# Performance work log

Measured on AMD Instinct MI355X. Metric: run time of the kernel, lower is better.

## Reference

```python
import jax, jax.numpy as jnp
import numpy as np

C = 256
RED = 8
CK = C // RED  # 32


def setup_inputs() -> dict:
    key = jax.random.key(0)
    ks = jax.random.split(key, 7)
    x = jax.random.normal(ks[0], (4, C, 64, 64), dtype=jnp.float32)
    s = 1.0 / np.sqrt(C)
    key_W = jax.random.uniform(ks[1], (CK, C), minval=-s, maxval=s, dtype=jnp.float32)
    key_b = jax.random.uniform(ks[2], (CK,), minval=-s, maxval=s, dtype=jnp.float32)
    query_W = jax.random.uniform(ks[3], (CK, C), minval=-s, maxval=s, dtype=jnp.float32)
    query_b = jax.random.uniform(ks[4], (CK,), minval=-s, maxval=s, dtype=jnp.float32)
    value_W = jax.random.uniform(ks[5], (C, C), minval=-s, maxval=s, dtype=jnp.float32)
    value_b = jax.random.uniform(ks[6], (C,), minval=-s, maxval=s, dtype=jnp.float32)
    alpha = jnp.zeros((1,), dtype=jnp.float32)
    return {"x": x, "key_W": key_W, "key_b": key_b, "query_W": query_W,
            "query_b": query_b, "value_W": value_W, "value_b": value_b,
            "alpha": alpha}


def reference(x, key_W, key_b, query_W, query_b, value_W, value_b, alpha):
    B, Cc, H, W = x.shape
    N = H * W
    xf = x.reshape(B, Cc, N)  # [B, C, N]
    # 1x1 convs == per-pixel linear projections
    k = jnp.einsum('kc,bcn->bkn', key_W, xf) + key_b[None, :, None]     # [B, CK, N]
    q = jnp.einsum('kc,bcn->bkn', query_W, xf) + query_b[None, :, None]  # [B, CK, N]
    v = jnp.einsum('oc,bcn->bon', value_W, xf) + value_b[None, :, None]  # [B, C, N]
    # energy[b, i, j] = key_i . query_j
    energy = jnp.einsum('bki,bkj->bij', k, q)  # [B, N, N]
    attn = jax.nn.softmax(energy, axis=-1)
    # out[b, c, i] = sum_j v[b, c, j] * attn[b, i, j]
    out = jnp.einsum('bcj,bij->bci', v, attn)  # [B, C, N]
    out = out.reshape(B, Cc, H, W)
    return alpha * out + x
```

## Files before the change

### kernel.cpp

```cpp
#include <hip/hip_runtime.h>

#define C_DIM 256
#define CK_DIM 32
#define NPIX 4096
#define BATCH 4

typedef __attribute__((ext_vector_type(8))) short bf16x8;
typedef __attribute__((ext_vector_type(4))) float f32x4;
typedef __attribute__((ext_vector_type(16))) float f32x16;
typedef __attribute__((ext_vector_type(4))) unsigned short us4;

__device__ __forceinline__ unsigned short f2bf(float f) {
    union { float f; unsigned int u; } c; c.f = f;
    unsigned int r = c.u + 0x7FFFu + ((c.u >> 16) & 1u);
    return (unsigned short)(r >> 16);
}

__global__ __launch_bounds__(256) void wprep_kernel(
    const float* __restrict__ kW, const float* __restrict__ qW,
    const float* __restrict__ vW, unsigned short* __restrict__ wbf)
{
    int i4 = (blockIdx.x * 256 + threadIdx.x) * 4;
    int o = i4 >> 8, c = i4 & 255;
    const float* src = (o < 32) ? kW + o * 256 + c
                     : (o < 64) ? qW + (o - 32) * 256 + c
                                : vW + (o - 64) * 256 + c;
    float4 f = *(const float4*)src;
    us4 p; p.x = f2bf(f.x); p.y = f2bf(f.y); p.z = f2bf(f.z); p.w = f2bf(f.w);
    *(us4*)&wbf[i4] = p;
}

#define XP 264
__global__ __launch_bounds__(256) void proj_kernel(
    const float* __restrict__ x,
    const unsigned short* __restrict__ wbf,
    const float* __restrict__ key_b, const float* __restrict__ query_b,
    const float* __restrict__ value_b,
    unsigned short* __restrict__ kT,
    unsigned short* __restrict__ qT,
    unsigned short* __restrict__ vt)
{
    const int b  = blockIdx.y;
    const int n0 = blockIdx.x * 64;
    const int t  = threadIdx.x;
    const int w    = t >> 6;
    const int lane = t & 63;
    const int mrow = lane & 15;
    const int quad = lane >> 4;

    __shared__ __align__(16) unsigned short smem[28928];
    #define XT(n, c)      smem[(n) * XP + (c)]
    #define VS(w_, c, nn) smem[(w_) * 6144 + (c) * 24 + (nn)]
    #define KQS(n, o)     smem[24576 + (n) * 68 + (o)]

    const float* xb = x + (size_t)b * C_DIM * NPIX + n0;
    const int cb = (t >> 4) * 4;
    const int n4 = (t & 15) * 4;
    #pragma unroll
    for (int it = 0; it < 4; ++it) {
        int c0 = it * 64 + cb;
        float4 r0 = *(const float4*)(xb + (size_t)(c0 + 0) * NPIX + n4);
        float4 r1 = *(const float4*)(xb + (size_t)(c0 + 1) * NPIX + n4);
        float4 r2 = *(const float4*)(xb + (size_t)(c0 + 2) * NPIX + n4);
        float4 r3 = *(const float4*)(xb + (size_t)(c0 + 3) * NPIX + n4);
        float d0[4] = {r0.x, r0.y, r0.z, r0.w};
        float d1[4] = {r1.x, r1.y, r1.z, r1.w};
        float d2[4] = {r2.x, r2.y, r2.z, r2.w};
        float d3[4] = {r3.x, r3.y, r3.z, r3.w};
        #pragma unroll
        for (int d = 0; d < 4; ++d) {
            us4 p; p.x = f2bf(d0[d]); p.y = f2bf(d1[d]);
                   p.z = f2bf(d2[d]); p.w = f2bf(d3[d]);
            *(us4*)&XT(n4 + d, c0) = p;
        }
    }
    __syncthreads();

    f32x4 acc[20];
    #pragma unroll
    for (int ot = 0; ot < 20; ++ot) acc[ot] = (f32x4){0.f, 0.f, 0.f, 0.f};

    const int ns = 16 * w;
    #pragma unroll
    for (int ck = 0; ck < 256; ck += 32) {
        bf16x8 bx = *(const bf16x8*)&XT(ns + mrow, ck + quad * 8);
        #pragma unroll
        for (int ot = 0; ot < 20; ++ot) {
            bf16x8 aw = *(const bf16x8*)(wbf + (size_t)(ot * 16 + mrow) * 256 + ck + quad * 8);
            acc[ot] = __builtin_amdgcn_mfma_f32_16x16x32_bf16(aw, bx, acc[ot], 0, 0, 0);
        }
    }
    __syncthreads();

    #pragma unroll
    for (int ot = 0; ot < 20; ++ot) {
        #pragma unroll
        for (int r = 0; r < 4; ++r) {
            int o = 16 * ot + 4 * quad + r;
            float bias = (ot < 2) ? key_b[o] : (ot < 4) ? query_b[o - 32] : value_b[o - 64];
            unsigned short val = f2bf(acc[ot][r] + bias);
            if (ot < 4) KQS(ns + mrow, o) = val;
            else        VS(w, o - 64, mrow) = val;
        }
    }
    __syncthreads();

    {
        int n = t >> 2, o8 = (t & 3) * 8;
        us4 pk = *(const us4*)&KQS(n, o8);
        us4 pq = *(const us4*)&KQS(n, 32 + o8);
        *(us4*)&kT[((size_t)b * NPIX + n0 + n) * CK_DIM + o8] = pk;
        *(us4*)&qT[((size_t)b * NPIX + n0 + n) * CK_DIM + o8] = pq;
    }
    {
        unsigned short* vbase = vt + ((size_t)b * (NPIX / 16) + n0 / 16 + w) * (C_DIM * 16);
        #pragma unroll
        for (int it = 0; it < 16; ++it) {
            int idx = it * 64 + lane;
            int c = idx >> 2, nn = (idx & 3) * 4;
            *(us4*)&vbase[c * 16 + nn] = *(const us4*)&VS(w, c, nn);
        }
    }
    #undef XT
    #undef VS
    #undef KQS
}

__global__ __launch_bounds__(256) void attn_kernel(
    const unsigned short* __restrict__ kT,
    const unsigned short* __restrict__ qT,
    const unsigned short* __restrict__ vt,
    const float* __restrict__ x, const float* __restrict__ alpha,
    float* __restrict__ out)
{
    const int b  = blockIdx.y;
    const int i0 = blockIdx.x * 32;
    const int t  = threadIdx.x;
    const int w    = t >> 6;
    const int lane = t & 63;
    const int mrow = lane & 15;
    const int quad = lane >> 4;
    const int m32  = lane & 31;
    const int half = lane >> 5;
    const int c0   = w * 64;

    __shared__ __align__(16) unsigned short Pt[2][32][136];
    __shared__ float lred[4][32];

    const unsigned short* kTb = kT + (size_t)b * NPIX * CK_DIM;
    const unsigned short* qTb = qT + (size_t)b * NPIX * CK_DIM;
    const unsigned short* vtb = vt + (size_t)b * (NPIX / 16) * (C_DIM * 16);

    bf16x8 kf[2];
    #pragma unroll
    for (int is = 0; is < 2; ++is)
        kf[is] = *(const bf16x8*)(kTb + (size_t)(i0 + 16 * is + mrow) * CK_DIM + quad * 8);

    f32x16 acc[2];
    #pragma unroll
    for (int cs = 0; cs < 2; ++cs)
        #pragma unroll
        for (int r = 0; r < 16; ++r) acc[cs][r] = 0.0f;

    float lacc[2] = {0.0f, 0.0f};
    int pp = 0;

    for (int jt = 0; jt < NPIX; jt += 128) {
        bf16x8 av[8][2];
        #pragma unroll
        for (int jb = 0; jb < 8; ++jb) {
            const unsigned short* vp = vtb + (size_t)(jt / 16 + jb) * (C_DIM * 16)
                                       + (size_t)(c0 + m32) * 16 + half * 8;
            av[jb][0] = *(const bf16x8*)vp;
            av[jb][1] = *(const bf16x8*)(vp + 32 * 16);
        }

        int jw = jt + 32 * w;
        #pragma unroll
        for (int js = 0; js < 2; ++js) {
            bf16x8 aq = *(const bf16x8*)(qTb + (size_t)(jw + 16 * js + mrow) * CK_DIM + quad * 8);
            #pragma unroll
            for (int is = 0; is < 2; ++is) {
                f32x4 d = __builtin_amdgcn_mfma_f32_16x16x32_bf16(
                    aq, kf[is], (f32x4){0.f, 0.f, 0.f, 0.f}, 0, 0, 0);
                float p0 = __expf(d[0]), p1 = __expf(d[1]);
                float p2 = __expf(d[2]), p3 = __expf(d[3]);
                lacc[is] += (p0 + p1) + (p2 + p3);
                us4 p;
                p.x = f2bf(p0); p.y = f2bf(p1); p.z = f2bf(p2); p.w = f2bf(p3);
                *(us4*)&Pt[pp][16 * is + mrow][32 * w + 16 * js + 4 * quad] = p;
            }
        }
        __syncthreads();

        #pragma unroll
        for (int jb = 0; jb < 8; ++jb) {
            bf16x8 bp = *(const bf16x8*)&Pt[pp][m32][16 * jb + half * 8];
            acc[0] = __builtin_amdgcn_mfma_f32_32x32x16_bf16(av[jb][0], bp, acc[0], 0, 0, 0);
            acc[1] = __builtin_amdgcn_mfma_f32_32x32x16_bf16(av[jb][1], bp, acc[1], 0, 0, 0);
        }
        pp ^= 1;
    }

    #pragma unroll
    for (int is = 0; is < 2; ++is) {
        lacc[is] += __shfl_xor(lacc[is], 16);
        lacc[is] += __shfl_xor(lacc[is], 32);
    }
    if (lane < 16) {
        #pragma unroll
        for (int is = 0; is < 2; ++is) lred[w][16 * is + lane] = lacc[is];
    }
    __syncthreads();

    const float al = alpha[0];
    float l = (lred[0][m32] + lred[1][m32]) + (lred[2][m32] + lred[3][m32]);
    float rs = al / l;

    const float* xb = x + (size_t)b * C_DIM * NPIX;
    float* ob = out + (size_t)b * C_DIM * NPIX;
    const int i = i0 + m32;
    #pragma unroll
    for (int cs = 0; cs < 2; ++cs)
        #pragma unroll
        for (int r = 0; r < 16; ++r) {
            int c = c0 + 32 * cs + (r & 3) + 8 * (r >> 2) + 4 * half;
            size_t idx = (size_t)c * NPIX + i;
            ob[idx] = acc[cs][r] * rs + xb[idx];
        }
}

extern "C" void kernel_launch(void* const* d_in, const int* in_sizes, int n_in,
                              void* d_out, int out_size, void* d_ws, size_t ws_size,
                              hipStream_t stream) {
    const float* x       = (const float*)d_in[0];
    const float* key_W   = (const float*)d_in[1];
    const float* key_b   = (const float*)d_in[2];
    const float* query_W = (const float*)d_in[3];
    const float* query_b = (const float*)d_in[4];
    const float* value_W = (const float*)d_in[5];
    const float* value_b = (const float*)d_in[6];
    const float* alpha   = (const float*)d_in[7];
    float* out = (float*)d_out;

    unsigned short* kT  = (unsigned short*)d_ws;
    unsigned short* qT  = kT + (size_t)BATCH * NPIX * CK_DIM;
    unsigned short* vt  = qT + (size_t)BATCH * NPIX * CK_DIM;
    unsigned short* wbf = vt + (size_t)BATCH * C_DIM * NPIX;

    wprep_kernel<<<80, 256, 0, stream>>>(key_W, query_W, value_W, wbf);

    dim3 gridA(NPIX / 64, BATCH);
    proj_kernel<<<gridA, 256, 0, stream>>>(x, wbf, key_b, query_b, value_b, kT, qT, vt);

    dim3 gridB(NPIX / 32, BATCH);
    attn_kernel<<<gridB, 256, 0, stream>>>(kT, qT, vt, x, alpha, out);
}
```

Before: 160.4 us.

## Enlarge attention query tile to 64 rows and halve projection tile per block

The attention kernel now handles 64 query rows per block instead of 32. Each loaded V fragment feeds twice as many MFMAs, which halves global V traffic per output, and the grid becomes a flat 256 blocks with a batch-interleaved mapping. The projection kernel now processes 32 pixels per block, with the 320 output channels split across wave pairs, to double block count and cut LDS use. The trade-off is more accumulator registers in attn (four 32x32 accumulators plus four key fragments), which may lower occupancy, and only 256 attention blocks, which may underfill the GPU.

```diff
diff --git a/kernel.cpp b/kernel.cpp
--- a/kernel.cpp
+++ b/kernel.cpp
@@ -41,24 +41,26 @@
     unsigned short* __restrict__ vt)
 {
     const int b  = blockIdx.y;
-    const int n0 = blockIdx.x * 64;
+    const int n0 = blockIdx.x * 32;
     const int t  = threadIdx.x;
     const int w    = t >> 6;
     const int lane = t & 63;
     const int mrow = lane & 15;
     const int quad = lane >> 4;
-
-    __shared__ __align__(16) unsigned short smem[28928];
-    #define XT(n, c)      smem[(n) * XP + (c)]
-    #define VS(w_, c, nn) smem[(w_) * 6144 + (c) * 24 + (nn)]
-    #define KQS(n, o)     smem[24576 + (n) * 68 + (o)]
+    const int oh   = w >> 1;
+    const int ns   = (w & 1) * 16;
+
+    __shared__ __align__(16) unsigned short smem[14592];
+    #define XT(n, c)       smem[(n) * XP + (c)]
+    #define VS(nsb, c, nn) smem[(nsb) * 6144 + (c) * 24 + (nn)]
+    #define KQS(n, o)      smem[12288 + (n) * 72 + (o)]
 
     const float* xb = x + (size_t)b * C_DIM * NPIX + n0;
-    const int cb = (t >> 4) * 4;
-    const int n4 = (t & 15) * 4;
-    #pragma unroll
-    for (int it = 0; it < 4; ++it) {
-        int c0 = it * 64 + cb;
+    const int cb = (t >> 3) * 4;
+    const int n4 = (t & 7) * 4;
+    #pragma unroll
+    for (int it = 0; it < 2; ++it) {
+        int c0 = it * 128 + cb;
         float4 r0 = *(const float4*)(xb + (size_t)(c0 + 0) * NPIX + n4);
         float4 r1 = *(const float4*)(xb + (size_t)(c0 + 1) * NPIX + n4);
         float4 r2 = *(const float4*)(xb + (size_t)(c0 + 2) * NPIX + n4);
@@ -76,50 +78,47 @@
     }
     __syncthreads();
 
-    f32x4 acc[20];
-    #pragma unroll
-    for (int ot = 0; ot < 20; ++ot) acc[ot] = (f32x4){0.f, 0.f, 0.f, 0.f};
-
-    const int ns = 16 * w;
-    #pragma unroll
+    f32x4 acc[10];
+    #pragma unroll
+    for (int ot = 0; ot < 10; ++ot) acc[ot] = (f32x4){0.f, 0.f, 0.f, 0.f};
+    const int obase = oh * 160;
+
+    #pragma unroll 2
     for (int ck = 0; ck < 256; ck += 32) {
         bf16x8 bx = *(const bf16x8*)&XT(ns + mrow, ck + quad * 8);
         #pragma unroll
-        for (int ot = 0; ot < 20; ++ot) {
-            bf16x8 aw = *(const bf16x8*)(wbf + (size_t)(ot * 16 + mrow) * 256 + ck + quad * 8);
+        for (int ot = 0; ot < 10; ++ot) {
+            bf16x8 aw = *(const bf16x8*)(wbf + (size_t)(obase + ot * 16 + mrow) * 256
+                                         + ck + quad * 8);
             acc[ot] = __builtin_amdgcn_mfma_f32_16x16x32_bf16(aw, bx, acc[ot], 0, 0, 0);
         }
     }
     __syncthreads();
 
     #pragma unroll
-    for (int ot = 0; ot < 20; ++ot) {
+    for (int ot = 0; ot < 10; ++ot) {
         #pragma unroll
         for (int r = 0; r < 4; ++r) {
-            int o = 16 * ot + 4 * quad + r;
-            float bias = (ot < 2) ? key_b[o] : (ot < 4) ? query_b[o - 32] : value_b[o - 64];
+            int o = obase + 16 * ot + 4 * quad + r;
+            float bias = (o < 32) ? key_b[o] : (o < 64) ? query_b[o - 32] : value_b[o - 64];
             unsigned short val = f2bf(acc[ot][r] + bias);
-            if (ot < 4) KQS(ns + mrow, o) = val;
-            else        VS(w, o - 64, mrow) = val;
+            if (o < 64) KQS(ns + mrow, o) = val;
+            else        VS(ns >> 4, o - 64, mrow) = val;
         }
     }
     __syncthreads();
 
     {
-        int n = t >> 2, o8 = (t & 3) * 8;
-        us4 pk = *(const us4*)&KQS(n, o8);
-        us4 pq = *(const us4*)&KQS(n, 32 + o8);
-        *(us4*)&kT[((size_t)b * NPIX + n0 + n) * CK_DIM + o8] = pk;
-        *(us4*)&qT[((size_t)b * NPIX + n0 + n) * CK_DIM + o8] = pq;
-    }
-    {
-        unsigned short* vbase = vt + ((size_t)b * (NPIX / 16) + n0 / 16 + w) * (C_DIM * 16);
-        #pragma unroll
-        for (int it = 0; it < 16; ++it) {
-            int idx = it * 64 + lane;
-            int c = idx >> 2, nn = (idx & 3) * 4;
-            *(us4*)&vbase[c * 16 + nn] = *(const us4*)&VS(w, c, nn);
-        }
+        int n = t >> 3, o4 = (t & 7) * 4;
+        *(us4*)&kT[((size_t)b * NPIX + n0 + n) * CK_DIM + o4] = *(const us4*)&KQS(n, o4);
+        *(us4*)&qT[((size_t)b * NPIX + n0 + n) * CK_DIM + o4] = *(const us4*)&KQS(n, 32 + o4);
+    }
+    #pragma unroll
+    for (int it = 0; it < 8; ++it) {
+        int flat = it * 256 + t;
+        int nsb = flat >> 10, c = (flat >> 2) & 255, nn = (flat & 3) * 4;
+        unsigned short* vbase = vt + ((size_t)b * (NPIX / 16) + n0 / 16 + nsb) * (C_DIM * 16);
+        *(us4*)&vbase[c * 16 + nn] = *(const us4*)&VS(nsb, c, nn);
     }
     #undef XT
     #undef VS
@@ -133,8 +132,9 @@
     const float* __restrict__ x, const float* __restrict__ alpha,
     float* __restrict__ out)
 {
-    const int b  = blockIdx.y;
-    const int i0 = blockIdx.x * 32;
+    const int f  = blockIdx.x;
+    const int b  = (f & 7) >> 1;
+    const int i0 = (((f >> 3) << 1) | (f & 1)) * 64;
     const int t  = threadIdx.x;
     const int w    = t >> 6;
     const int lane = t & 63;
@@ -144,25 +144,27 @@
     const int half = lane >> 5;
     const int c0   = w * 64;
 
-    __shared__ __align__(16) unsigned short Pt[2][32][136];
-    __shared__ float lred[4][32];
+    __shared__ __align__(16) unsigned short Pt[2][64][136];
+    __shared__ float lred[4][64];
 
     const unsigned short* kTb = kT + (size_t)b * NPIX * CK_DIM;
     const unsigned short* qTb = qT + (size_t)b * NPIX * CK_DIM;
     const unsigned short* vtb = vt + (size_t)b * (NPIX / 16) * (C_DIM * 16);
 
-    bf16x8 kf[2];
-    #pragma unroll
-    for (int is = 0; is < 2; ++is)
+    bf16x8 kf[4];
+    #pragma unroll
+    for (int is = 0; is < 4; ++is)
         kf[is] = *(const bf16x8*)(kTb + (size_t)(i0 + 16 * is + mrow) * CK_DIM + quad * 8);
 
-    f32x16 acc[2];
+    f32x16 acc[2][2];
     #pragma unroll
     for (int cs = 0; cs < 2; ++cs)
         #pragma unroll
-        for (int r = 0; r < 16; ++r) acc[cs][r] = 0.0f;
-
-    float lacc[2] = {0.0f, 0.0f};
+        for (int ih = 0; ih < 2; ++ih)
+            #pragma unroll
+            for (int r = 0; r < 16; ++r) acc[cs][ih][r] = 0.0f;
+
+    float lacc[4] = {0.f, 0.f, 0.f, 0.f};
     int pp = 0;
 
     for (int jt = 0; jt < NPIX; jt += 128) {
@@ -180,7 +182,7 @@
         for (int js = 0; js < 2; ++js) {
             bf16x8 aq = *(const bf16x8*)(qTb + (size_t)(jw + 16 * js + mrow) * CK_DIM + quad * 8);
             #pragma unroll
-            for (int is = 0; is < 2; ++is) {
+            for (int is = 0; is < 4; ++is) {
                 f32x4 d = __builtin_amdgcn_mfma_f32_16x16x32_bf16(
                     aq, kf[is], (f32x4){0.f, 0.f, 0.f, 0.f}, 0, 0, 0);
                 float p0 = __expf(d[0]), p1 = __expf(d[1]);
@@ -195,38 +197,49 @@
 
         #pragma unroll
         for (int jb = 0; jb < 8; ++jb) {
-            bf16x8 bp = *(const bf16x8*)&Pt[pp][m32][16 * jb + half * 8];
-            acc[0] = __builtin_amdgcn_mfma_f32_32x32x16_bf16(av[jb][0], bp, acc[0], 0, 0, 0);
-            acc[1] = __builtin_amdgcn_mfma_f32_32x32x16_bf16(av[jb][1], bp, acc[1], 0, 0, 0);
+            bf16x8 bp0 = *(const bf16x8*)&Pt[pp][m32][16 * jb + half * 8];
+            bf16x8 bp1 = *(const bf16x8*)&Pt[pp][32 + m32][16 * jb + half * 8];
+            acc[0][0] = __builtin_amdgcn_mfma_f32_32x32x16_bf16(av[jb][0], bp0, acc[0][0], 0, 0, 0);
+            acc[1][0] = __builtin_amdgcn_mfma_f32_32x32x16_bf16(av[jb][1], bp0, acc[1][0], 0, 0, 0);
+            acc[0][1] = __builtin_amdgcn_mfma_f32_32x32x16_bf16(av[jb][0], bp1, acc[0][1], 0, 0, 0);
+            acc[1][1] = __builtin_amdgcn_mfma_f32_32x32x16_bf16(av[jb][1], bp1, acc[1][1], 0, 0, 0);
         }
         pp ^= 1;
     }
 
     #pragma unroll
-    for (int is = 0; is < 2; ++is) {
+    for (int is = 0; is < 4; ++is) {
         lacc[is] += __shfl_xor(lacc[is], 16);
         lacc[is] += __shfl_xor(lacc[is], 32);
     }
     if (lane < 16) {
         #pragma unroll
-        for (int is = 0; is < 2; ++is) lred[w][16 * is + lane] = lacc[is];
+        for (int is = 0; is < 4; ++is) lred[w][16 * is + lane] = lacc[is];
     }
     __syncthreads();
 
     const float al = alpha[0];
-    float l = (lred[0][m32] + lred[1][m32]) + (lred[2][m32] + lred[3][m32]);
-    float rs = al / l;
+    float rs[2];
+    #pragma unroll
+    for (int ih = 0; ih < 2; ++ih) {
+        int li = 32 * ih + m32;
+        float l = (lred[0][li] + lred[1][li]) + (lred[2][li] + lred[3][li]);
+        rs[ih] = al / l;
+    }
 
     const float* xb = x + (size_t)b * C_DIM * NPIX;
     float* ob = out + (size_t)b * C_DIM * NPIX;
-    const int i = i0 + m32;
     #pragma unroll
     for (int cs = 0; cs < 2; ++cs)
         #pragma unroll
-        for (int r = 0; r < 16; ++r) {
-            int c = c0 + 32 * cs + (r & 3) + 8 * (r >> 2) + 4 * half;
-            size_t idx = (size_t)c * NPIX + i;
-            ob[idx] = acc[cs][r] * rs + xb[idx];
+        for (int ih = 0; ih < 2; ++ih) {
+            int i = i0 + 32 * ih + m32;
+            #pragma unroll
+            for (int r = 0; r < 16; ++r) {
+                int c = c0 + 32 * cs + (r & 3) + 8 * (r >> 2) + 4 * half;
+                size_t idx = (size_t)c * NPIX + i;
+                ob[idx] = acc[cs][ih][r] * rs[ih] + xb[idx];
+            }
         }
 }
 
@@ -250,9 +263,8 @@
 
     wprep_kernel<<<80, 256, 0, stream>>>(key_W, query_W, value_W, wbf);
 
-    dim3 gridA(NPIX / 64, BATCH);
+    dim3 gridA(NPIX / 32, BATCH);
     proj_kernel<<<gridA, 256, 0, stream>>>(x, wbf, key_b, query_b, value_b, kT, qT, vt);
 
-    dim3 gridB(NPIX / 32, BATCH);
-    attn_kernel<<<gridB, 256, 0, stream>>>(kT, qT, vt, x, alpha, out);
-}
+    attn_kernel<<<256, 256, 0, stream>>>(kT, qT, vt, x, alpha, out);
+}
```

Result: no change. 162.4 us (+1.3%).
